# Optimization experiments

Hardware: AMD Instinct MI355X
Metric: run time of the kernel (lower is better)

## Reference

```python
import jax, jax.numpy as jnp
import numpy as np

WIN = (7, 7)
N_HEADS = 4
DIM = 128


def _relative_pos_index(win):
    h, w = win
    coords = np.stack(np.meshgrid(np.arange(h), np.arange(w), indexing='ij'))  # [2,h,w]
    flat = coords.reshape(2, -1)  # [2, h*w]
    rel = flat[:, :, None] - flat[:, None, :]  # [2, N, N]
    rel = rel.transpose(1, 2, 0)
    rel[:, :, 0] += h - 1
    rel[:, :, 1] += w - 1
    rel[:, :, 0] *= 2 * w - 1
    return rel.sum(-1).astype(np.int64)  # [N, N]


def setup_inputs() -> dict:
    key = jax.random.key(0)
    ks = jax.random.split(key, 6)
    B_, N, C = 4096, WIN[0] * WIN[1], DIM
    nW = 64
    table_len = (2 * WIN[0] - 1) * (2 * WIN[1] - 1)  # 169
    return {
        'x': jax.random.normal(ks[0], (B_, N, C), dtype=jnp.float32),
        'mask': jnp.zeros((nW, N, N), dtype=jnp.float32),
        'qkv_w': jax.random.normal(ks[1], (C, 3 * C), dtype=jnp.float32) * 0.02,
        'qkv_b': jnp.zeros((3 * C,), dtype=jnp.float32),
        'proj_w': jax.random.normal(ks[2], (C, C), dtype=jnp.float32) * 0.02,
        'proj_b': jnp.zeros((C,), dtype=jnp.float32),
        'bias_table': jax.random.normal(ks[3], (table_len, N_HEADS), dtype=jnp.float32) * 0.02,
        'rel_index': jnp.asarray(_relative_pos_index(WIN)),  # [N, N] int64
    }


def reference(x, mask, qkv_w, qkv_b, proj_w, proj_b, bias_table, rel_index):
    B_, N, C = x.shape
    H = N_HEADS
    hd = C // H
    scale = hd ** (-0.5)
    # qkv projection -> [3, B_, H, N, hd]
    qkv = (x @ qkv_w + qkv_b).reshape(B_, N, 3, H, hd).transpose(2, 0, 3, 1, 4)
    q, k, v = qkv[0] * scale, qkv[1], qkv[2]
    attn = jnp.einsum('bhnd,bhmd->bhnm', q, k)  # [B_, H, N, N]
    # gathered relative position bias -> [H, N, N]
    bias = bias_table[rel_index.reshape(-1)].reshape(N, N, H).transpose(2, 0, 1)
    attn = attn + bias[None]
    nW = mask.shape[0]
    attn = attn.reshape(-1, nW, H, N, N) + mask[None, :, None, :, :]
    attn = jax.nn.softmax(attn.reshape(-1, H, N, N), axis=-1)
    out = jnp.einsum('bhnm,bhmd->bhnd', attn, v)  # [B_, H, N, hd]
    out = out.transpose(0, 2, 1, 3).reshape(B_, N, C)
    return out @ proj_w + proj_b
```

## Files before the change

### kernel.cpp

```cpp
#include <hip/hip_runtime.h>
#include <hip/hip_bf16.h>

typedef __bf16 bf16x8 __attribute__((ext_vector_type(8)));
typedef __bf16 bf16x4 __attribute__((ext_vector_type(4)));
typedef float f32x4 __attribute__((ext_vector_type(4)));

#define MFMA16(a, b, c) __builtin_amdgcn_mfma_f32_16x16x32_bf16((a), (b), (c), 0, 0, 0)

constexpr int kB = 4096, kN = 49, kC = 128;
constexpr float kScale = 0.17677669529663687f;
constexpr float kLog2e = 1.4426950408889634f;
constexpr float kQScale = kScale * kLog2e;

constexpr size_t WQ_OFF = 0;
constexpr size_t WP_OFF = 98304;
constexpr size_t BP_OFF = 131072;
constexpr size_t MF_OFF = 196608;

__global__ void prep_kernel(const float* __restrict__ qkv_w,
                            const float* __restrict__ proj_w,
                            const float* __restrict__ bias_table,
                            const int* __restrict__ rel_raw,
                            const float* __restrict__ maskp,
                            __bf16* __restrict__ wq, __bf16* __restrict__ wp,
                            float* __restrict__ biasp, int* __restrict__ mf) {
  const int blk = blockIdx.x, t = threadIdx.x;
  const bool is64 = (rel_raw[1] == 0);
  if (blk < 16) {
    const int kk = t >> 6, lane = t & 63, lm = lane & 15;
    const int k0 = kk * 32 + ((lane >> 4) << 3);
    const int qk = blk >> 3, head = (blk >> 1) & 3, dt = blk & 1;
    const int c = qk * 128 + head * 32 + ((lm >> 2) << 3) + dt * 4 + (lm & 3);
    const float s = (qk == 0) ? kQScale : 1.f;
#pragma unroll
    for (int i = 0; i < 8; ++i)
      wq[((blk * 4 + kk) * 64 + lane) * 8 + i] =
          (__bf16)(qkv_w[(k0 + i) * 384 + c] * s);
  } else if (blk < 24) {
    const int kk = t >> 6, lane = t & 63;
    const int k0 = kk * 32 + ((lane >> 4) << 3);
    const int c  = blk * 16 + (lane & 15);
#pragma unroll
    for (int i = 0; i < 8; ++i)
      wq[((blk * 4 + kk) * 64 + lane) * 8 + i] = (__bf16)qkv_w[(k0 + i) * 384 + c];
  } else if (blk < 32) {
    const int nt = blk - 24;
    const int kk = t >> 6, lane = t & 63, lm = lane & 15;
    const int k0 = kk * 32 + ((lane >> 4) << 3);
    const int c = (nt >> 1) * 32 + 2 * lm + (nt & 1);
#pragma unroll
    for (int i = 0; i < 8; ++i)
      wp[((nt * 4 + kk) * 64 + lane) * 8 + i] = (__bf16)proj_w[(k0 + i) * 128 + c];
  } else if (blk < 96) {
    const int e = (blk - 32) * 256 + t;
    const int h = e >> 12, tok = (e >> 6) & 63, key = e & 63;
    float v;
    if (key >= kN) v = -1e30f;
    else if (tok >= kN) v = 0.f;
    else {
      const int flat = tok * kN + key;
      const int idx = is64 ? rel_raw[2 * flat] : rel_raw[flat];
      v = bias_table[idx * 4 + h] * kLog2e;
    }
    biasp[(h * 64 + tok) * 64 + key] = v;
  } else {
    const int base = (blk - 96) * 19208;
    int any = 0;
    for (int e = base + t; e < base + 19208; e += 256)
      any |= (__float_as_uint(maskp[e]) != 0u) ? 1 : 0;
    const int blkany = __syncthreads_or(any);
    if (t == 0) mf[blk - 96] = blkany;
  }
}

__device__ __forceinline__ uint2 pack4(f32x4 v) {
  bf16x4 h;
  h[0] = (__bf16)v[0]; h[1] = (__bf16)v[1]; h[2] = (__bf16)v[2]; h[3] = (__bf16)v[3];
  return *(uint2*)&h;
}

__device__ __forceinline__ bf16x8 cat2(uint2 a, uint2 b) {
  uint4 u;
  u.x = a.x; u.y = a.y; u.z = b.x; u.w = b.y;
  return *(bf16x8*)&u;
}

__global__ __launch_bounds__(256, 4)
void wattn_fused(const float* __restrict__ x, const float* __restrict__ qkv_b,
                 const float* __restrict__ proj_b,
                 const __bf16* __restrict__ wq, const __bf16* __restrict__ wp,
                 const float* __restrict__ biasp, const float* __restrict__ mask,
                 const int* __restrict__ mf, float* __restrict__ out) {
  constexpr int XS = 136, OBS = 136;
  __shared__ __align__(16) __bf16 xb[64 * XS];
  __bf16* ob = xb;

  const int tid = threadIdx.x;
  const int w = tid >> 6, lane = tid & 63, lg = lane >> 4, lm = lane & 15;
  const int b = blockIdx.x;
  const f32x4 zero4 = {0.f, 0.f, 0.f, 0.f};

  const bool hasMask =
      (mf[0] | mf[1] | mf[2] | mf[3] | mf[4] | mf[5] | mf[6] | mf[7]) != 0;

  {
    const float* xp = x + (size_t)b * (kN * kC);
#pragma unroll
    for (int i = 0; i < 8; ++i) {
      const int it = tid + i * 256;
      const int row = it >> 5, col = (it & 31) << 2;
      const int sr = row < kN ? row : (kN - 1);
      f32x4 v = *(const f32x4*)(xp + sr * kC + col);
      bf16x4 h;
      h[0] = (__bf16)v[0]; h[1] = (__bf16)v[1]; h[2] = (__bf16)v[2]; h[3] = (__bf16)v[3];
      *(bf16x4*)(xb + row * XS + col) = h;
    }
  }
  __syncthreads();

#define LDAF(tt, kk) (*(const bf16x8*)(xb + ((tt) * 16 + lm) * XS + (kk) * 32 + lg * 8))

  bf16x8 qf[4], kf[4], vf[2][2];

  {
    bf16x8 wf[2][4];
    f32x4 qb4[2];
#pragma unroll
    for (int dt = 0; dt < 2; ++dt) {
      const int ct = 2 * w + dt;
#pragma unroll
      for (int kk = 0; kk < 4; ++kk)
        wf[dt][kk] = *(const bf16x8*)(wq + ((size_t)(ct * 4 + kk) * 64 + lane) * 8);
      qb4[dt] = *(const f32x4*)(qkv_b + w * 32 + lg * 8 + dt * 4);
#pragma unroll
      for (int j = 0; j < 4; ++j) qb4[dt][j] *= kQScale;
    }
#pragma unroll
    for (int tt = 0; tt < 4; ++tt) {
      bf16x8 af_t[4];
#pragma unroll
      for (int kk = 0; kk < 4; ++kk) af_t[kk] = LDAF(tt, kk);
      uint2 qh[2];
#pragma unroll
      for (int dt = 0; dt < 2; ++dt) {
        f32x4 acc = zero4;
        __builtin_amdgcn_s_setprio(1);
#pragma unroll
        for (int kk = 0; kk < 4; ++kk) acc = MFMA16(wf[dt][kk], af_t[kk], acc);
        __builtin_amdgcn_s_setprio(0);
#pragma unroll
        for (int j = 0; j < 4; ++j) acc[j] += qb4[dt][j];
        qh[dt] = pack4(acc);
      }
      qf[tt] = cat2(qh[0], qh[1]);
    }
  }

  {
    bf16x8 wf[2][4];
    f32x4 kb4[2];
#pragma unroll
    for (int dt = 0; dt < 2; ++dt) {
      const int ct = 8 + 2 * w + dt;
#pragma unroll
      for (int kk = 0; kk < 4; ++kk)
        wf[dt][kk] = *(const bf16x8*)(wq + ((size_t)(ct * 4 + kk) * 64 + lane) * 8);
      kb4[dt] = *(const f32x4*)(qkv_b + 128 + w * 32 + lg * 8 + dt * 4);
    }
#pragma unroll
    for (int tt = 0; tt < 4; ++tt) {
      bf16x8 af_t[4];
#pragma unroll
      for (int kk = 0; kk < 4; ++kk) af_t[kk] = LDAF(tt, kk);
      uint2 kh[2];
#pragma unroll
      for (int dt = 0; dt < 2; ++dt) {
        f32x4 acc = zero4;
        __builtin_amdgcn_s_setprio(1);
#pragma unroll
        for (int kk = 0; kk < 4; ++kk) acc = MFMA16(wf[dt][kk], af_t[kk], acc);
        __builtin_amdgcn_s_setprio(0);
#pragma unroll
        for (int j = 0; j < 4; ++j) acc[j] += kb4[dt][j];
        kh[dt] = pack4(acc);
      }
      kf[tt] = cat2(kh[0], kh[1]);
    }
  }

  {
    bf16x8 wf[2][4];
    float vb[2];
#pragma unroll
    for (int dt = 0; dt < 2; ++dt) {
      const int ct = 16 + 2 * w + dt;
#pragma unroll
      for (int kk = 0; kk < 4; ++kk)
        wf[dt][kk] = *(const bf16x8*)(wq + ((size_t)(ct * 4 + kk) * 64 + lane) * 8);
      vb[dt] = qkv_b[256 + w * 32 + dt * 16 + lm];
    }
    uint2 vh[2][2];
#pragma unroll
    for (int mt = 0; mt < 4; ++mt) {
      bf16x8 af_t[4];
#pragma unroll
      for (int kk = 0; kk < 4; ++kk) af_t[kk] = LDAF(mt, kk);
#pragma unroll
      for (int dt = 0; dt < 2; ++dt) {
        f32x4 acc = zero4;
        __builtin_amdgcn_s_setprio(1);
#pragma unroll
        for (int kk = 0; kk < 4; ++kk) acc = MFMA16(af_t[kk], wf[dt][kk], acc);
        __builtin_amdgcn_s_setprio(0);
#pragma unroll
        for (int j = 0; j < 4; ++j) acc[j] += vb[dt];
        vh[mt & 1][dt] = pack4(acc);
      }
      if (mt & 1) {
#pragma unroll
        for (int dt = 0; dt < 2; ++dt)
          vf[mt >> 1][dt] = cat2(vh[0][dt], vh[1][dt]);
      }
    }
  }
  __syncthreads();

  const float* bpp = biasp + w * 4096;
  const float* mkp = mask + (size_t)(b & 63) * (kN * kN);

#pragma unroll
  for (int tt = 0; tt < 4; ++tt) {
    f32x4 st[4];
    __builtin_amdgcn_s_setprio(1);
#pragma unroll
    for (int kt = 0; kt < 4; ++kt) st[kt] = MFMA16(kf[kt], qf[tt], zero4);
    __builtin_amdgcn_s_setprio(0);
    const int tok = tt * 16 + lm;
#pragma unroll
    for (int kt = 0; kt < 4; ++kt) {
      f32x4 bm = *(const f32x4*)(bpp + (tok << 6) + kt * 16 + lg * 4);
#pragma unroll
      for (int j = 0; j < 4; ++j) st[kt][j] += bm[j];
    }
    if (hasMask) {
      const int tok2 = tok < kN ? tok : (kN - 1);
#pragma unroll
      for (int kt = 0; kt < 4; ++kt)
#pragma unroll
        for (int j = 0; j < 4; ++j) {
          const int key = kt * 16 + lg * 4 + j;
          const int key2 = key < kN ? key : (kN - 1);
          st[kt][j] += mkp[tok2 * kN + key2] * kLog2e;
        }
    }
    float m = -3e38f;
#pragma unroll
    for (int kt = 0; kt < 4; ++kt)
#pragma unroll
      for (int j = 0; j < 4; ++j) m = fmaxf(m, st[kt][j]);
    m = fmaxf(m, __shfl_xor(m, 16));
    m = fmaxf(m, __shfl_xor(m, 32));
    float sum = 0.f;
#pragma unroll
    for (int kt = 0; kt < 4; ++kt)
#pragma unroll
      for (int j = 0; j < 4; ++j) {
        const float e = exp2f(st[kt][j] - m);
        st[kt][j] = e;
        sum += e;
      }
    sum += __shfl_xor(sum, 16);
    sum += __shfl_xor(sum, 32);
    const float rs = __builtin_amdgcn_rcpf(sum);
    uint2 pst[4];
#pragma unroll
    for (int kt = 0; kt < 4; ++kt) {
      f32x4 t;
#pragma unroll
      for (int j = 0; j < 4; ++j) t[j] = st[kt][j] * rs;
      pst[kt] = pack4(t);
    }
    bf16x8 pa0 = cat2(pst[0], pst[1]);
    bf16x8 pa1 = cat2(pst[2], pst[3]);
#pragma unroll
    for (int dt = 0; dt < 2; ++dt) {
      f32x4 o = MFMA16(pa0, vf[0][dt], zero4);
      o = MFMA16(pa1, vf[1][dt], o);
#pragma unroll
      for (int j = 0; j < 4; ++j)
        ob[(tt * 16 + lg * 4 + j) * OBS + w * 32 + dt * 16 + lm] = (__bf16)o[j];
    }
  }

  bf16x8 wpb[2][4];
#pragma unroll
  for (int n = 0; n < 2; ++n)
#pragma unroll
    for (int kk = 0; kk < 4; ++kk)
      wpb[n][kk] = *(const bf16x8*)(wp + (size_t)(((w * 2 + n) * 4 + kk) * 64 + lane) * 8);

  __syncthreads();

  {
    float* op = out + (size_t)b * (kN * kC);
    const float pb0 = proj_b[w * 32 + 2 * lm];
    const float pb1 = proj_b[w * 32 + 2 * lm + 1];
#pragma unroll
    for (int mt = 0; mt < 4; ++mt) {
      bf16x8 paf[4];
#pragma unroll
      for (int kk = 0; kk < 4; ++kk)
        paf[kk] = *(const bf16x8*)(ob + (mt * 16 + lm) * OBS + kk * 32 + lg * 8);
      f32x4 a0 = zero4, a1 = zero4;
      __builtin_amdgcn_s_setprio(1);
#pragma unroll
      for (int kk = 0; kk < 4; ++kk) {
        a0 = MFMA16(paf[kk], wpb[0][kk], a0);
        a1 = MFMA16(paf[kk], wpb[1][kk], a1);
      }
      __builtin_amdgcn_s_setprio(0);
#pragma unroll
      for (int j = 0; j < 4; ++j) {
        const int r = mt * 16 + lg * 4 + j;
        if (r < kN) {
          float2 st2;
          st2.x = a0[j] + pb0;
          st2.y = a1[j] + pb1;
          *(float2*)(op + r * kC + w * 32 + 2 * lm) = st2;
        }
      }
    }
  }
#undef LDAF
}

extern "C" void kernel_launch(void* const* d_in, const int* in_sizes, int n_in,
                              void* d_out, int out_size, void* d_ws, size_t ws_size,
                              hipStream_t stream) {
  const float* x          = (const float*)d_in[0];
  const float* mask       = (const float*)d_in[1];
  const float* qkv_w      = (const float*)d_in[2];
  const float* qkv_b      = (const float*)d_in[3];
  const float* proj_w     = (const float*)d_in[4];
  const float* proj_b     = (const float*)d_in[5];
  const float* bias_table = (const float*)d_in[6];
  const int*   rel        = (const int*)d_in[7];

  char* ws = (char*)d_ws;
  __bf16* wq   = (__bf16*)(ws + WQ_OFF);
  __bf16* wp   = (__bf16*)(ws + WP_OFF);
  float* biasp = (float*)(ws + BP_OFF);
  int*   mf    = (int*)(ws + MF_OFF);

  prep_kernel<<<104, 256, 0, stream>>>(qkv_w, proj_w, bias_table, rel, mask,
                                       wq, wp, biasp, mf);
  wattn_fused<<<kB, 256, 0, stream>>>(x, qkv_b, proj_b, wq, wp, biasp, mask,
                                      mf, (float*)d_out);
}
```

Before: 103.5 us.

## Spill V fragments to LDS, swizzle shared layout, fold biases into MFMA accumulators

Moves the per-wave V fragments out of registers into a dedicated LDS region and reloads them during the PV MFMA. This frees registers so launch bounds can rise from 4 to 5 waves-groups per SM. The x/out staging buffer switches from a padded row stride to an XOR-swizzled 256-byte row layout to avoid bank conflicts. QKV biases now initialise the accumulators instead of being added afterward. Shared memory grows to 32 KB per block and the extra LDS reads of V could offset the occupancy gain.

```diff
diff --git a/kernel.cpp b/kernel.cpp
--- a/kernel.cpp
+++ b/kernel.cpp
@@ -85,15 +85,15 @@
   return *(bf16x8*)&u;
 }
 
-__global__ __launch_bounds__(256, 4)
+__global__ __launch_bounds__(256, 5)
 void wattn_fused(const float* __restrict__ x, const float* __restrict__ qkv_b,
                  const float* __restrict__ proj_b,
                  const __bf16* __restrict__ wq, const __bf16* __restrict__ wp,
                  const float* __restrict__ biasp, const float* __restrict__ mask,
                  const int* __restrict__ mf, float* __restrict__ out) {
-  constexpr int XS = 136, OBS = 136;
-  __shared__ __align__(16) __bf16 xb[64 * XS];
-  __bf16* ob = xb;
+  __shared__ __align__(16) char smem[32768];
+  char* xb  = smem;
+  char* vls = smem + 16384;
 
   const int tid = threadIdx.x;
   const int w = tid >> 6, lane = tid & 63, lg = lane >> 4, lm = lane & 15;
@@ -108,19 +108,22 @@
 #pragma unroll
     for (int i = 0; i < 8; ++i) {
       const int it = tid + i * 256;
-      const int row = it >> 5, col = (it & 31) << 2;
+      const int row = it >> 5;
+      const int colB = (it & 31) * 8;
       const int sr = row < kN ? row : (kN - 1);
-      f32x4 v = *(const f32x4*)(xp + sr * kC + col);
+      f32x4 v = *(const f32x4*)(xp + sr * kC + (it & 31) * 4);
       bf16x4 h;
       h[0] = (__bf16)v[0]; h[1] = (__bf16)v[1]; h[2] = (__bf16)v[2]; h[3] = (__bf16)v[3];
-      *(bf16x4*)(xb + row * XS + col) = h;
+      *(bf16x4*)(xb + (((row << 8) + colB) ^ ((row & 7) << 4))) = h;
     }
   }
   __syncthreads();
 
-#define LDAF(tt, kk) (*(const bf16x8*)(xb + ((tt) * 16 + lm) * XS + (kk) * 32 + lg * 8))
-
-  bf16x8 qf[4], kf[4], vf[2][2];
+#define LDAF(t16, kk)                                                          \
+  (*(const bf16x8*)(xb + (((((t16) * 16 + lm) << 8) + (kk) * 64 + lg * 16) ^   \
+                          ((lm & 7) << 4))))
+
+  bf16x8 qf[4], kf[4];
 
   {
     bf16x8 wf[2][4];
@@ -143,13 +146,11 @@
       uint2 qh[2];
 #pragma unroll
       for (int dt = 0; dt < 2; ++dt) {
-        f32x4 acc = zero4;
+        f32x4 acc = qb4[dt];
         __builtin_amdgcn_s_setprio(1);
 #pragma unroll
         for (int kk = 0; kk < 4; ++kk) acc = MFMA16(wf[dt][kk], af_t[kk], acc);
         __builtin_amdgcn_s_setprio(0);
-#pragma unroll
-        for (int j = 0; j < 4; ++j) acc[j] += qb4[dt][j];
         qh[dt] = pack4(acc);
       }
       qf[tt] = cat2(qh[0], qh[1]);
@@ -175,13 +176,11 @@
       uint2 kh[2];
 #pragma unroll
       for (int dt = 0; dt < 2; ++dt) {
-        f32x4 acc = zero4;
+        f32x4 acc = kb4[dt];
         __builtin_amdgcn_s_setprio(1);
 #pragma unroll
         for (int kk = 0; kk < 4; ++kk) acc = MFMA16(wf[dt][kk], af_t[kk], acc);
         __builtin_amdgcn_s_setprio(0);
-#pragma unroll
-        for (int j = 0; j < 4; ++j) acc[j] += kb4[dt][j];
         kh[dt] = pack4(acc);
       }
       kf[tt] = cat2(kh[0], kh[1]);
@@ -189,6 +188,7 @@
   }
 
   {
+    char* vbw = vls + w * 4096;
     bf16x8 wf[2][4];
     float vb[2];
 #pragma unroll
@@ -207,19 +207,18 @@
       for (int kk = 0; kk < 4; ++kk) af_t[kk] = LDAF(mt, kk);
 #pragma unroll
       for (int dt = 0; dt < 2; ++dt) {
-        f32x4 acc = zero4;
+        f32x4 acc = {vb[dt], vb[dt], vb[dt], vb[dt]};
         __builtin_amdgcn_s_setprio(1);
 #pragma unroll
         for (int kk = 0; kk < 4; ++kk) acc = MFMA16(af_t[kk], wf[dt][kk], acc);
         __builtin_amdgcn_s_setprio(0);
-#pragma unroll
-        for (int j = 0; j < 4; ++j) acc[j] += vb[dt];
         vh[mt & 1][dt] = pack4(acc);
       }
       if (mt & 1) {
 #pragma unroll
         for (int dt = 0; dt < 2; ++dt)
-          vf[mt >> 1][dt] = cat2(vh[0][dt], vh[1][dt]);
+          *(bf16x8*)(vbw + (((mt >> 1) * 2 + dt) * 64 + lane) * 16) =
+              cat2(vh[0][dt], vh[1][dt]);
       }
     }
   }
@@ -227,6 +226,7 @@
 
   const float* bpp = biasp + w * 4096;
   const float* mkp = mask + (size_t)(b & 63) * (kN * kN);
+  const char* vbw = vls + w * 4096;
 
 #pragma unroll
   for (int tt = 0; tt < 4; ++tt) {
@@ -284,11 +284,16 @@
     bf16x8 pa1 = cat2(pst[2], pst[3]);
 #pragma unroll
     for (int dt = 0; dt < 2; ++dt) {
-      f32x4 o = MFMA16(pa0, vf[0][dt], zero4);
-      o = MFMA16(pa1, vf[1][dt], o);
-#pragma unroll
-      for (int j = 0; j < 4; ++j)
-        ob[(tt * 16 + lg * 4 + j) * OBS + w * 32 + dt * 16 + lm] = (__bf16)o[j];
+      bf16x8 v0 = *(const bf16x8*)(vbw + ((0 + dt) * 64 + lane) * 16);
+      bf16x8 v1 = *(const bf16x8*)(vbw + ((2 + dt) * 64 + lane) * 16);
+      f32x4 o = MFMA16(pa0, v0, zero4);
+      o = MFMA16(pa1, v1, o);
+#pragma unroll
+      for (int j = 0; j < 4; ++j) {
+        const int r = tt * 16 + lg * 4 + j;
+        const int colB = (w * 32 + dt * 16 + lm) * 2;
+        *(__bf16*)(xb + (((r << 8) + colB) ^ ((r & 7) << 4))) = (__bf16)o[j];
+      }
     }
   }
 
@@ -309,8 +314,7 @@
     for (int mt = 0; mt < 4; ++mt) {
       bf16x8 paf[4];
 #pragma unroll
-      for (int kk = 0; kk < 4; ++kk)
-        paf[kk] = *(const bf16x8*)(ob + (mt * 16 + lm) * OBS + kk * 32 + lg * 8);
+      for (int kk = 0; kk < 4; ++kk) paf[kk] = LDAF(mt, kk);
       f32x4 a0 = zero4, a1 = zero4;
       __builtin_amdgcn_s_setprio(1);
 #pragma unroll
```

After: 209.1 us. 102% more time.
